# Performance work log

Hardware: AMD Instinct MI355X
Metric: run time of the kernel (lower is better)

The kernel has to match this reference:

```python
import jax, jax.numpy as jnp
import numpy as np

N_NODES = 100000
N_EDGES = 1600000
D_IN = 64
D_OUT = 64


def setup_inputs() -> dict:
    key = jax.random.key(0)
    k1, k2, k3, k4, k5, k6 = jax.random.split(key, 6)
    feat = jax.random.normal(k1, (N_NODES, D_IN), dtype=jnp.float32)
    src = jax.random.randint(k2, (N_EDGES,), 0, N_NODES, dtype=jnp.int64)
    dst = jax.random.randint(k3, (N_EDGES,), 0, N_NODES, dtype=jnp.int64)
    edge_weight = jax.random.uniform(k4, (N_EDGES,), dtype=jnp.float32)
    # Xavier-uniform with relu gain, as in reset_parameters
    gain = float(np.sqrt(2.0))
    bound = gain * float(np.sqrt(6.0 / (D_IN + D_OUT)))
    W_neigh = jax.random.uniform(k5, (D_OUT, D_IN), dtype=jnp.float32, minval=-bound, maxval=bound)
    W_self = jax.random.uniform(k6, (D_OUT, D_IN), dtype=jnp.float32, minval=-bound, maxval=bound)
    bias = jnp.zeros((D_OUT,), dtype=jnp.float32)
    return {"feat": feat, "src": src, "dst": dst, "edge_weight": edge_weight,
            "W_neigh": W_neigh, "W_self": W_self, "bias": bias}


def reference(feat, src, dst, edge_weight, W_neigh, W_self, bias):
    n = feat.shape[0]
    # feat_drop with p=0.0 is identity; in_feats == out_feats so lin_before_mp is False
    # message: u_mul_e -> gather src features, scale by edge weight  [E, D_IN]
    m = feat[src] * edge_weight[:, None]
    # mean reduce over incoming edges (zero for isolated dst nodes, matching DGL)
    s = jax.ops.segment_sum(m, dst, num_segments=n)
    deg = jax.ops.segment_sum(jnp.ones_like(edge_weight), dst, num_segments=n)
    neigh = s / jnp.maximum(deg, 1.0)[:, None]
    h_neigh = neigh @ W_neigh.T
    h_self = feat @ W_self.T
    return h_self + h_neigh + bias
```

## Files before the change

kernel.cpp:

```cpp
#include <hip/hip_runtime.h>
#include <hip/hip_fp16.h>

constexpr int N_NODES = 100000;
constexpr int N_EDGES = 1600000;
constexpr int D = 64;

constexpr int BSH    = 6;
constexpr int BN     = 1 << BSH;
constexpr int NBUCK  = (N_NODES + BN - 1) / BN;
constexpr int NN2    = NBUCK * BN;
constexpr int NCNTB  = 800;
constexpr int EPB2   = N_EDGES / NCNTB;
constexpr int NCVT   = (N_NODES * D / 4) / 256;
constexpr int NSB    = (NN2 + 1 + 1023) / 1024;
constexpr int NBINS  = (NN2 + 1023) >> 10;
constexpr int CHUNK  = 2048;
constexpr int NPA    = (N_EDGES + CHUNK - 1) / CHUNK;

constexpr size_t OFF_NCNT     = 0;
constexpr size_t OFF_NSTART   = 400384;
constexpr size_t OFF_BINCNT   = 800768;
constexpr size_t OFF_BINSTART = 801280;
constexpr size_t OFF_BINCUR   = 801792;
constexpr size_t OFF_TMP      = 1201152;
constexpr size_t OFF_BSUM     = 1601536;
constexpr size_t OFF_W16      = 1602048;
constexpr size_t OFF_FEAT16   = 1634816;
constexpr size_t OFF_ENT2     = OFF_FEAT16 + (size_t)N_NODES * D * 2;
constexpr size_t OFF_ENTA     = OFF_ENT2 + (size_t)N_EDGES * 8;
constexpr size_t WS_NEEDED    = OFF_ENTA + (size_t)N_EDGES * 8;

typedef short  bf16x8 __attribute__((ext_vector_type(8)));
typedef float  f32x4  __attribute__((ext_vector_type(4)));

__device__ __forceinline__ unsigned short f2bf(float f) {
    unsigned u = __float_as_uint(f);
    u += 0x7fffu + ((u >> 16) & 1u);
    return (unsigned short)(u >> 16);
}

__device__ __forceinline__ float h2f_lo(unsigned u) {
    return __half2float(__ushort_as_half((unsigned short)(u & 0xFFFFu)));
}
__device__ __forceinline__ float h2f_hi(unsigned u) {
    return __half2float(__ushort_as_half((unsigned short)(u >> 16)));
}

__device__ __forceinline__ void split8(float4 p0, float4 p1, bf16x8& hi, bf16x8& lo) {
    float f[8] = {p0.x, p0.y, p0.z, p0.w, p1.x, p1.y, p1.z, p1.w};
#pragma unroll
    for (int i = 0; i < 8; ++i) {
        const unsigned short h = f2bf(f[i]);
        const float hf = __uint_as_float((unsigned)h << 16);
        hi[i] = (short)h;
        lo[i] = (short)f2bf(f[i] - hf);
    }
}

__global__ __launch_bounds__(256) void k_zero(int* __restrict__ bincnt) {
    int i = blockIdx.x * 256 + threadIdx.x;
    if (i < NBINS) bincnt[i] = 0;
}

__global__ __launch_bounds__(256) void k_pre(const float4* __restrict__ feat4,
                                             unsigned short* __restrict__ feat16,
                                             const float* __restrict__ Wn,
                                             const float* __restrict__ Ws,
                                             unsigned short* __restrict__ W16,
                                             const int* __restrict__ dst,
                                             int* __restrict__ bincnt) {
    __shared__ int l[NBINS];
    const int b   = blockIdx.x;
    const int tid = threadIdx.x;
    if (b < NCVT) {
        const int i = b * 256 + tid;
        float4 v = feat4[i];
        ushort4 o;
        o.x = __half_as_ushort(__float2half_rn(v.x));
        o.y = __half_as_ushort(__float2half_rn(v.y));
        o.z = __half_as_ushort(__float2half_rn(v.z));
        o.w = __half_as_ushort(__float2half_rn(v.w));
        *(ushort4*)&feat16[(size_t)i * 4] = o;
    } else if (b < NCVT + NCNTB) {
        for (int i = tid; i < NBINS; i += 256) l[i] = 0;
        __syncthreads();
        const int base = (b - NCVT) * EPB2;
        for (int k = tid; k < EPB2; k += 256)
            atomicAdd(&l[dst[base + k] >> 10], 1);
        __syncthreads();
        for (int i = tid; i < NBINS; i += 256)
            if (l[i]) atomicAdd(&bincnt[i], l[i]);
    } else {
        for (int e = tid; e < D * 128; e += 256) {
            const int j = e >> 7, k = e & 127;
            const float w = (k < D) ? Ws[j * D + k] : Wn[j * D + (k - D)];
            const unsigned short h = f2bf(w);
            const float hf = __uint_as_float((unsigned)h << 16);
            W16[e] = h;
            W16[D * 128 + e] = f2bf(w - hf);
        }
    }
}

__global__ __launch_bounds__(128) void k_scan_bins(const int* __restrict__ bincnt,
                                                   int* __restrict__ binstart,
                                                   int* __restrict__ bincur) {
    __shared__ int s[128];
    const int t = threadIdx.x;
    const int v = (t < NBINS) ? bincnt[t] : 0;
    s[t] = v;
    __syncthreads();
    for (int off = 1; off < 128; off <<= 1) {
        int u = (t >= off) ? s[t - off] : 0;
        __syncthreads();
        s[t] += u;
        __syncthreads();
    }
    if (t < NBINS) { binstart[t] = s[t] - v; bincur[t] = s[t] - v; }
    if (t == 0) binstart[NBINS] = N_EDGES;
}

__global__ __launch_bounds__(256) void k_place_a(const int* __restrict__ src,
                                                 const int* __restrict__ dst,
                                                 const float* __restrict__ ew,
                                                 int* __restrict__ bincur,
                                                 uint2* __restrict__ entriesA) {
    __shared__ __align__(16) uint2 stage[CHUNK];
    __shared__ unsigned char sbin[CHUNK];
    __shared__ int hist[NBINS], lstart[NBINS], lcur[NBINS], gbase[NBINS];
    __shared__ int s[256];
    const int tid = threadIdx.x;
    const int e0  = blockIdx.x * CHUNK;
    const int cnt = min(CHUNK, N_EDGES - e0);

    for (int i = tid; i < NBINS; i += 256) hist[i] = 0;
    __syncthreads();
    for (int k = tid; k < cnt; k += 256)
        atomicAdd(&hist[dst[e0 + k] >> 10], 1);
    __syncthreads();
    {
        const int v = (tid < NBINS) ? hist[tid] : 0;
        s[tid] = v;
        __syncthreads();
        for (int off = 1; off < 256; off <<= 1) {
            int u = (tid >= off) ? s[tid - off] : 0;
            __syncthreads();
            s[tid] += u;
            __syncthreads();
        }
        if (tid < NBINS) {
            const int ex = s[tid] - v;
            lstart[tid] = ex;
            lcur[tid]   = ex;
            gbase[tid]  = v ? atomicAdd(&bincur[tid], v) : 0;
        }
    }
    __syncthreads();
    for (int k = tid; k < cnt; k += 256) {
        const int d = dst[e0 + k];
        const int b = d >> 10;
        const int p = atomicAdd(&lcur[b], 1);
        stage[p] = make_uint2((unsigned)src[e0 + k] | ((unsigned)(d & 1023) << 17),
                              __float_as_uint(ew[e0 + k]));
        sbin[p]  = (unsigned char)b;
    }
    __syncthreads();
    for (int j = tid; j < cnt; j += 256) {
        const int b = sbin[j];
        entriesA[gbase[b] + (j - lstart[b])] = stage[j];
    }
}

__global__ __launch_bounds__(1024) void k_hist(const int* __restrict__ binstart,
                                               const uint2* __restrict__ entriesA,
                                               int* __restrict__ ncnt) {
    __shared__ int h[1024];
    const int tid = threadIdx.x;
    const int b   = blockIdx.x;
    h[tid] = 0;
    __syncthreads();
    const int s0  = binstart[b];
    const int cnt = binstart[b + 1] - s0;
    for (int k = tid; k < cnt; k += 1024)
        atomicAdd(&h[entriesA[s0 + k].x >> 17], 1);
    __syncthreads();
    const int n = (b << 10) + tid;
    if (n < NN2) ncnt[n] = h[tid];
}

__global__ __launch_bounds__(1024) void k_scan_a(const int* __restrict__ ncnt,
                                                 int* __restrict__ tmp,
                                                 int* __restrict__ bsum) {
    __shared__ int s[1024];
    const int t   = threadIdx.x;
    const int gid = blockIdx.x * 1024 + t;
    const int v   = (gid < NN2) ? ncnt[gid] : 0;
    s[t] = v;
    __syncthreads();
    for (int off = 1; off < 1024; off <<= 1) {
        int u = (t >= off) ? s[t - off] : 0;
        __syncthreads();
        s[t] += u;
        __syncthreads();
    }
    if (gid <= NN2) tmp[gid] = s[t] - v;
    if (t == 1023) bsum[blockIdx.x] = s[t];
}

__global__ __launch_bounds__(128) void k_scan_b(int* __restrict__ bsum) {
    __shared__ int s[128];
    const int t = threadIdx.x;
    const int v = (t < NSB) ? bsum[t] : 0;
    s[t] = v;
    __syncthreads();
    for (int off = 1; off < 128; off <<= 1) {
        int u = (t >= off) ? s[t - off] : 0;
        __syncthreads();
        s[t] += u;
        __syncthreads();
    }
    if (t < NSB) bsum[t] = s[t] - v;
}

__global__ __launch_bounds__(1024) void k_scan_c(const int* __restrict__ tmp,
                                                 const int* __restrict__ bsum,
                                                 int* __restrict__ nstart) {
    const int gid = blockIdx.x * 1024 + threadIdx.x;
    if (gid <= NN2) nstart[gid] = tmp[gid] + bsum[blockIdx.x];
}

__global__ __launch_bounds__(1024) void k_place_b(const int* __restrict__ binstart,
                                                  const uint2* __restrict__ entriesA,
                                                  const int* __restrict__ nstart,
                                                  uint2* __restrict__ entries2) {
    __shared__ int cur[1024];
    const int tid = threadIdx.x;
    const int b   = blockIdx.x;
    const int n0  = b << 10;
    const int nn  = min(1024, NN2 - n0);
    if (tid < nn) cur[tid] = nstart[n0 + tid];
    __syncthreads();
    const int s0  = binstart[b];
    const int cnt = binstart[b + 1] - s0;
    for (int k = tid; k < cnt; k += 1024) {
        const uint2 a = entriesA[s0 + k];
        const int p = atomicAdd(&cur[a.x >> 17], 1);
        entries2[p] = make_uint2(a.x & 0x1FFFFu, a.y);
    }
}

__global__ __launch_bounds__(256, 8) void k_bucket(
    const uint2* __restrict__ feat16u2,
    const float* __restrict__ feat32,
    const int* __restrict__ nstart,
    const uint2* __restrict__ entries2,
    const unsigned short* __restrict__ W16,
    const float* __restrict__ bias,
    float* __restrict__ out) {
    __shared__ __align__(16) float aggrow[BN * 68];
    __shared__ int hh[BN], st[BN];
    const int tid = threadIdx.x;
    const int b   = blockIdx.x;

    if (tid < BN) {
        const int s = nstart[b * BN + tid];
        const int e = nstart[b * BN + tid + 1];
        st[tid] = s;
        hh[tid] = e - s;
    }
    __syncthreads();

    const int wave = tid >> 6, lane = tid & 63;
    const int group = lane >> 4, gl = lane & 15;
    for (int t = 0; t < 16; ++t) {
        const int dl  = wave * 16 + t;
        const int ss  = st[dl];
        const int deg = hh[dl];
        const int se  = ss + deg;
        float4 acc = make_float4(0.f, 0.f, 0.f, 0.f);
        int e = ss + group;
        for (; e + 4 < se; e += 8) {
            const uint2 en0 = entries2[e];
            const uint2 en1 = entries2[e + 4];
            const uint2 p0  = feat16u2[(size_t)en0.x * 16 + gl];
            const uint2 p1  = feat16u2[(size_t)en1.x * 16 + gl];
            const float w0  = __uint_as_float(en0.y);
            const float w1  = __uint_as_float(en1.y);
            acc.x = fmaf(h2f_lo(p0.x), w0, acc.x);
            acc.y = fmaf(h2f_hi(p0.x), w0, acc.y);
            acc.z = fmaf(h2f_lo(p0.y), w0, acc.z);
            acc.w = fmaf(h2f_hi(p0.y), w0, acc.w);
            acc.x = fmaf(h2f_lo(p1.x), w1, acc.x);
            acc.y = fmaf(h2f_hi(p1.x), w1, acc.y);
            acc.z = fmaf(h2f_lo(p1.y), w1, acc.z);
            acc.w = fmaf(h2f_hi(p1.y), w1, acc.w);
        }
        if (e < se) {
            const uint2 en = entries2[e];
            const float w  = __uint_as_float(en.y);
            const uint2 p  = feat16u2[(size_t)en.x * 16 + gl];
            acc.x = fmaf(h2f_lo(p.x), w, acc.x);
            acc.y = fmaf(h2f_hi(p.x), w, acc.y);
            acc.z = fmaf(h2f_lo(p.y), w, acc.z);
            acc.w = fmaf(h2f_hi(p.y), w, acc.w);
        }
#pragma unroll
        for (int m = 16; m <= 32; m <<= 1) {
            acc.x += __shfl_xor(acc.x, m);
            acc.y += __shfl_xor(acc.y, m);
            acc.z += __shfl_xor(acc.z, m);
            acc.w += __shfl_xor(acc.w, m);
        }
        if (group == 0) {
            const float inv = 1.0f / fmaxf((float)deg, 1.0f);
            float4 o = make_float4(acc.x * inv, acc.y * inv, acc.z * inv, acc.w * inv);
            *(float4*)&aggrow[dl * 68 + gl * 4] = o;
        }
    }
    __syncthreads();

    const int quad = lane >> 4, r = lane & 15;
    const int node0 = b * BN + wave * 16;
    int arow = node0 + r;
    if (arow > N_NODES - 1) arow = N_NODES - 1;

    bf16x8 ahi[4], alo[4];
    {
        const float* fp = &feat32[(size_t)arow * 64 + quad * 8];
        split8(*(const float4*)fp,        *(const float4*)(fp + 4),  ahi[0], alo[0]);
        split8(*(const float4*)(fp + 32), *(const float4*)(fp + 36), ahi[1], alo[1]);
        const float* ap = &aggrow[(wave * 16 + r) * 68 + quad * 8];
        split8(*(const float4*)ap,        *(const float4*)(ap + 4),  ahi[2], alo[2]);
        split8(*(const float4*)(ap + 32), *(const float4*)(ap + 36), ahi[3], alo[3]);
    }

    const unsigned short* W16lo = W16 + D * 128;
    f32x4 acc4[4] = {};
#pragma unroll
    for (int nt = 0; nt < 4; ++nt) {
#pragma unroll
        for (int kc = 0; kc < 4; ++kc) {
            const size_t wo = (size_t)(nt * 16 + r) * 128 + kc * 32 + quad * 8;
            const bf16x8 bhi = *(const bf16x8*)&W16[wo];
            const bf16x8 blo = *(const bf16x8*)&W16lo[wo];
            acc4[nt] = __builtin_amdgcn_mfma_f32_16x16x32_bf16(ahi[kc], bhi, acc4[nt], 0, 0, 0);
            acc4[nt] = __builtin_amdgcn_mfma_f32_16x16x32_bf16(alo[kc], bhi, acc4[nt], 0, 0, 0);
            acc4[nt] = __builtin_amdgcn_mfma_f32_16x16x32_bf16(ahi[kc], blo, acc4[nt], 0, 0, 0);
        }
    }

#pragma unroll
    for (int nt = 0; nt < 4; ++nt) {
        const float bv = bias[nt * 16 + r];
#pragma unroll
        for (int reg = 0; reg < 4; ++reg) {
            const int m = node0 + quad * 4 + reg;
            if (m < N_NODES) out[(size_t)m * 64 + nt * 16 + r] = acc4[nt][reg] + bv;
        }
    }
}

__global__ __launch_bounds__(256) void fb_zero(float4* __restrict__ out4,
                                               float* __restrict__ deg) {
    const int stride = gridDim.x * blockDim.x;
    int i = blockIdx.x * blockDim.x + threadIdx.x;
    const int total4 = (N_NODES * D) / 4;
    for (int idx = i; idx < total4; idx += stride)
        out4[idx] = make_float4(0.f, 0.f, 0.f, 0.f);
    for (int idx = i; idx < N_NODES; idx += stride)
        deg[idx] = 0.f;
}

__global__ __launch_bounds__(256) void fb_scatter(
    const float* __restrict__ feat, const int* __restrict__ src,
    const int* __restrict__ dst, const float* __restrict__ ew,
    float* __restrict__ out, float* __restrict__ deg) {
    const int gid  = blockIdx.x * blockDim.x + threadIdx.x;
    const int e    = gid >> 6;
    const int lane = gid & 63;
    if (e >= N_EDGES) return;
    atomicAdd(&out[(size_t)dst[e] * D + lane], feat[(size_t)src[e] * D + lane] * ew[e]);
    if (lane == 0) atomicAdd(&deg[dst[e]], 1.0f);
}

__global__ __launch_bounds__(256) void fb_finalize(
    const float* __restrict__ feat, const float* __restrict__ Wn,
    const float* __restrict__ Ws, const float* __restrict__ bias,
    const float* __restrict__ deg, float* __restrict__ out) {
    __shared__ float lWn[D * 65];
    __shared__ float lWs[D * 65];
    for (int idx = threadIdx.x; idx < D * D; idx += 256) {
        const int r = idx >> 6, c = idx & 63;
        lWn[r * 65 + c] = Wn[idx];
        lWs[r * 65 + c] = Ws[idx];
    }
    __syncthreads();
    const int wave = threadIdx.x >> 6;
    const int lane = threadIdx.x & 63;
    const int n = blockIdx.x * 4 + wave;
    if (n >= N_NODES) return;
    const float f  = feat[(size_t)n * D + lane];
    const float sv = out[(size_t)n * D + lane];
    const float inv = 1.0f / fmaxf(deg[n], 1.0f);
    float acc_s = 0.f, acc_n = 0.f;
#pragma unroll
    for (int k = 0; k < D; ++k) {
        acc_s += __shfl(f, k)  * lWs[lane * 65 + k];
        acc_n += __shfl(sv, k) * lWn[lane * 65 + k];
    }
    out[(size_t)n * D + lane] = acc_s + acc_n * inv + bias[lane];
}

extern "C" void kernel_launch(void* const* d_in, const int* in_sizes, int n_in,
                              void* d_out, int out_size, void* d_ws, size_t ws_size,
                              hipStream_t stream) {
    const float* feat = (const float*)d_in[0];
    const int*   src  = (const int*)  d_in[1];
    const int*   dst  = (const int*)  d_in[2];
    const float* ew   = (const float*)d_in[3];
    const float* Wn   = (const float*)d_in[4];
    const float* Ws   = (const float*)d_in[5];
    const float* bias = (const float*)d_in[6];
    float* out = (float*)d_out;
    char* ws = (char*)d_ws;

    if (ws_size >= WS_NEEDED) {
        int* ncnt     = (int*)(ws + OFF_NCNT);
        int* nstart   = (int*)(ws + OFF_NSTART);
        int* bincnt   = (int*)(ws + OFF_BINCNT);
        int* binstart = (int*)(ws + OFF_BINSTART);
        int* bincur   = (int*)(ws + OFF_BINCUR);
        int* tmp      = (int*)(ws + OFF_TMP);
        int* bsum     = (int*)(ws + OFF_BSUM);
        unsigned short* W16    = (unsigned short*)(ws + OFF_W16);
        unsigned short* feat16 = (unsigned short*)(ws + OFF_FEAT16);
        uint2* entries2 = (uint2*)(ws + OFF_ENT2);
        uint2* entriesA = (uint2*)(ws + OFF_ENTA);

        k_zero     <<<1, 256, 0, stream>>>(bincnt);
        k_pre      <<<NCVT + NCNTB + 1, 256, 0, stream>>>((const float4*)feat, feat16,
                                                          Wn, Ws, W16, dst, bincnt);
        k_scan_bins<<<1, 128, 0, stream>>>(bincnt, binstart, bincur);
        k_place_a  <<<NPA, 256, 0, stream>>>(src, dst, ew, bincur, entriesA);
        k_hist     <<<NBINS, 1024, 0, stream>>>(binstart, entriesA, ncnt);
        k_scan_a   <<<NSB, 1024, 0, stream>>>(ncnt, tmp, bsum);
        k_scan_b   <<<1, 128, 0, stream>>>(bsum);
        k_scan_c   <<<NSB, 1024, 0, stream>>>(tmp, bsum, nstart);
        k_place_b  <<<NBINS, 1024, 0, stream>>>(binstart, entriesA, nstart, entries2);
        k_bucket   <<<NBUCK, 256, 0, stream>>>((const uint2*)feat16, feat, nstart,
                                               entries2, W16, bias, out);
    } else {
        float* deg = (float*)d_ws;
        fb_zero<<<2048, 256, 0, stream>>>((float4*)out, deg);
        fb_scatter<<<(N_EDGES * 64) / 256, 256, 0, stream>>>(feat, src, dst, ew, out, deg);
        fb_finalize<<<(N_NODES + 3) / 4, 256, 0, stream>>>(feat, Wn, Ws, bias, deg, out);
    }
}
```

Measured before the change: 246.5 us.

## Fuse per-bin histogram, scan and placement into one kernel; unroll gather loop deeper

Replaces the five-kernel sequence (histogram, three-phase global scan, placement) with a single per-bin kernel. It histograms node counts in shared memory, does a local exclusive scan offset by the bin's global start, writes nstart, and places the entries. This removes four launches and the global round trips through the ncnt, tmp and bsum buffers. Separately, the edge-gather loop in k_bucket is unrolled from 2 to 4 edges per lane, with a loop for the remainder, to expose more memory-level parallelism at the cost of extra registers.

```diff
diff --git a/kernel.cpp b/kernel.cpp
--- a/kernel.cpp
+++ b/kernel.cpp
@@ -12,18 +12,14 @@
 constexpr int NCNTB  = 800;
 constexpr int EPB2   = N_EDGES / NCNTB;
 constexpr int NCVT   = (N_NODES * D / 4) / 256;
-constexpr int NSB    = (NN2 + 1 + 1023) / 1024;
 constexpr int NBINS  = (NN2 + 1023) >> 10;
 constexpr int CHUNK  = 2048;
 constexpr int NPA    = (N_EDGES + CHUNK - 1) / CHUNK;
 
-constexpr size_t OFF_NCNT     = 0;
 constexpr size_t OFF_NSTART   = 400384;
 constexpr size_t OFF_BINCNT   = 800768;
 constexpr size_t OFF_BINSTART = 801280;
 constexpr size_t OFF_BINCUR   = 801792;
-constexpr size_t OFF_TMP      = 1201152;
-constexpr size_t OFF_BSUM     = 1601536;
 constexpr size_t OFF_W16      = 1602048;
 constexpr size_t OFF_FEAT16   = 1634816;
 constexpr size_t OFF_ENT2     = OFF_FEAT16 + (size_t)N_NODES * D * 2;
@@ -171,77 +167,38 @@
     }
 }
 
-__global__ __launch_bounds__(1024) void k_hist(const int* __restrict__ binstart,
-                                               const uint2* __restrict__ entriesA,
-                                               int* __restrict__ ncnt) {
+__global__ __launch_bounds__(1024) void k_sortbin(const int* __restrict__ binstart,
+                                                  const uint2* __restrict__ entriesA,
+                                                  int* __restrict__ nstart,
+                                                  uint2* __restrict__ entries2) {
     __shared__ int h[1024];
-    const int tid = threadIdx.x;
-    const int b   = blockIdx.x;
-    h[tid] = 0;
-    __syncthreads();
-    const int s0  = binstart[b];
-    const int cnt = binstart[b + 1] - s0;
-    for (int k = tid; k < cnt; k += 1024)
-        atomicAdd(&h[entriesA[s0 + k].x >> 17], 1);
-    __syncthreads();
-    const int n = (b << 10) + tid;
-    if (n < NN2) ncnt[n] = h[tid];
-}
-
-__global__ __launch_bounds__(1024) void k_scan_a(const int* __restrict__ ncnt,
-                                                 int* __restrict__ tmp,
-                                                 int* __restrict__ bsum) {
     __shared__ int s[1024];
-    const int t   = threadIdx.x;
-    const int gid = blockIdx.x * 1024 + t;
-    const int v   = (gid < NN2) ? ncnt[gid] : 0;
-    s[t] = v;
-    __syncthreads();
-    for (int off = 1; off < 1024; off <<= 1) {
-        int u = (t >= off) ? s[t - off] : 0;
-        __syncthreads();
-        s[t] += u;
-        __syncthreads();
-    }
-    if (gid <= NN2) tmp[gid] = s[t] - v;
-    if (t == 1023) bsum[blockIdx.x] = s[t];
-}
-
-__global__ __launch_bounds__(128) void k_scan_b(int* __restrict__ bsum) {
-    __shared__ int s[128];
-    const int t = threadIdx.x;
-    const int v = (t < NSB) ? bsum[t] : 0;
-    s[t] = v;
-    __syncthreads();
-    for (int off = 1; off < 128; off <<= 1) {
-        int u = (t >= off) ? s[t - off] : 0;
-        __syncthreads();
-        s[t] += u;
-        __syncthreads();
-    }
-    if (t < NSB) bsum[t] = s[t] - v;
-}
-
-__global__ __launch_bounds__(1024) void k_scan_c(const int* __restrict__ tmp,
-                                                 const int* __restrict__ bsum,
-                                                 int* __restrict__ nstart) {
-    const int gid = blockIdx.x * 1024 + threadIdx.x;
-    if (gid <= NN2) nstart[gid] = tmp[gid] + bsum[blockIdx.x];
-}
-
-__global__ __launch_bounds__(1024) void k_place_b(const int* __restrict__ binstart,
-                                                  const uint2* __restrict__ entriesA,
-                                                  const int* __restrict__ nstart,
-                                                  uint2* __restrict__ entries2) {
     __shared__ int cur[1024];
     const int tid = threadIdx.x;
     const int b   = blockIdx.x;
-    const int n0  = b << 10;
-    const int nn  = min(1024, NN2 - n0);
-    if (tid < nn) cur[tid] = nstart[n0 + tid];
-    __syncthreads();
     const int s0  = binstart[b];
     const int cnt = binstart[b + 1] - s0;
+
+    h[tid] = 0;
+    __syncthreads();
+    for (int k = tid; k < cnt; k += 1024)
+        atomicAdd(&h[entriesA[s0 + k].x >> 17], 1);
+    __syncthreads();
+    const int v = h[tid];
+    s[tid] = v;
+    __syncthreads();
+    for (int off = 1; off < 1024; off <<= 1) {
+        int u = (tid >= off) ? s[tid - off] : 0;
+        __syncthreads();
+        s[tid] += u;
+        __syncthreads();
+    }
+    const int pos = s0 + s[tid] - v;
+    cur[tid] = pos;
+    const int n = (b << 10) + tid;
+    if (n < NN2) nstart[n] = pos;
+    if (b == NBINS - 1 && tid == 0) nstart[NN2] = N_EDGES;
+    __syncthreads();
     for (int k = tid; k < cnt; k += 1024) {
         const uint2 a = entriesA[s0 + k];
         const int p = atomicAdd(&cur[a.x >> 17], 1);
@@ -279,13 +236,19 @@
         const int se  = ss + deg;
         float4 acc = make_float4(0.f, 0.f, 0.f, 0.f);
         int e = ss + group;
-        for (; e + 4 < se; e += 8) {
+        for (; e + 12 < se; e += 16) {
             const uint2 en0 = entries2[e];
             const uint2 en1 = entries2[e + 4];
+            const uint2 en2 = entries2[e + 8];
+            const uint2 en3 = entries2[e + 12];
             const uint2 p0  = feat16u2[(size_t)en0.x * 16 + gl];
             const uint2 p1  = feat16u2[(size_t)en1.x * 16 + gl];
+            const uint2 p2  = feat16u2[(size_t)en2.x * 16 + gl];
+            const uint2 p3  = feat16u2[(size_t)en3.x * 16 + gl];
             const float w0  = __uint_as_float(en0.y);
             const float w1  = __uint_as_float(en1.y);
+            const float w2  = __uint_as_float(en2.y);
+            const float w3  = __uint_as_float(en3.y);
             acc.x = fmaf(h2f_lo(p0.x), w0, acc.x);
             acc.y = fmaf(h2f_hi(p0.x), w0, acc.y);
             acc.z = fmaf(h2f_lo(p0.y), w0, acc.z);
@@ -294,8 +257,16 @@
             acc.y = fmaf(h2f_hi(p1.x), w1, acc.y);
             acc.z = fmaf(h2f_lo(p1.y), w1, acc.z);
             acc.w = fmaf(h2f_hi(p1.y), w1, acc.w);
-        }
-        if (e < se) {
+            acc.x = fmaf(h2f_lo(p2.x), w2, acc.x);
+            acc.y = fmaf(h2f_hi(p2.x), w2, acc.y);
+            acc.z = fmaf(h2f_lo(p2.y), w2, acc.z);
+            acc.w = fmaf(h2f_hi(p2.y), w2, acc.w);
+            acc.x = fmaf(h2f_lo(p3.x), w3, acc.x);
+            acc.y = fmaf(h2f_hi(p3.x), w3, acc.y);
+            acc.z = fmaf(h2f_lo(p3.y), w3, acc.z);
+            acc.w = fmaf(h2f_hi(p3.y), w3, acc.w);
+        }
+        for (; e < se; e += 4) {
             const uint2 en = entries2[e];
             const float w  = __uint_as_float(en.y);
             const uint2 p  = feat16u2[(size_t)en.x * 16 + gl];
@@ -425,13 +396,10 @@
     char* ws = (char*)d_ws;
 
     if (ws_size >= WS_NEEDED) {
-        int* ncnt     = (int*)(ws + OFF_NCNT);
         int* nstart   = (int*)(ws + OFF_NSTART);
         int* bincnt   = (int*)(ws + OFF_BINCNT);
         int* binstart = (int*)(ws + OFF_BINSTART);
         int* bincur   = (int*)(ws + OFF_BINCUR);
-        int* tmp      = (int*)(ws + OFF_TMP);
-        int* bsum     = (int*)(ws + OFF_BSUM);
         unsigned short* W16    = (unsigned short*)(ws + OFF_W16);
         unsigned short* feat16 = (unsigned short*)(ws + OFF_FEAT16);
         uint2* entries2 = (uint2*)(ws + OFF_ENT2);
@@ -442,11 +410,7 @@
                                                           Wn, Ws, W16, dst, bincnt);
         k_scan_bins<<<1, 128, 0, stream>>>(bincnt, binstart, bincur);
         k_place_a  <<<NPA, 256, 0, stream>>>(src, dst, ew, bincur, entriesA);
-        k_hist     <<<NBINS, 1024, 0, stream>>>(binstart, entriesA, ncnt);
-        k_scan_a   <<<NSB, 1024, 0, stream>>>(ncnt, tmp, bsum);
-        k_scan_b   <<<1, 128, 0, stream>>>(bsum);
-        k_scan_c   <<<NSB, 1024, 0, stream>>>(tmp, bsum, nstart);
-        k_place_b  <<<NBINS, 1024, 0, stream>>>(binstart, entriesA, nstart, entries2);
+        k_sortbin  <<<NBINS, 1024, 0, stream>>>(binstart, entriesA, nstart, entries2);
         k_bucket   <<<NBUCK, 256, 0, stream>>>((const uint2*)feat16, feat, nstart,
                                                entries2, W16, bias, out);
     } else {
```

New measurement: 246.4 us. About the same (-0.0%).
